# Kernel tuning notes

Measured on AMD Instinct MI355X. Metric: run time of the kernel, lower is better.

## Reference

```python
import jax, jax.numpy as jnp
import numpy as np

N = 102400   # total nodes (64 graphs x 1600 nodes)
G = 64       # graphs in batch
NPG = N // G
E = 1638400  # total edges (avg degree 16)
EPG = E // G


def _segmean(x, ids, num):
    s = jax.ops.segment_sum(x, ids, num_segments=num)
    c = jax.ops.segment_sum(jnp.ones((x.shape[0], 1), x.dtype), ids, num_segments=num)
    return s / jnp.maximum(c, 1.0)


def setup_inputs() -> dict:
    key = jax.random.key(0)
    ks = jax.random.split(key, 32)
    node_features = jax.random.normal(ks[0], (N, 60), jnp.float32)
    edge_features = jax.random.normal(ks[1], (E, 1), jnp.float32)
    node_graph = jnp.arange(N, dtype=jnp.int32) // NPG
    edge_graph = jnp.arange(E, dtype=jnp.int32) // EPG
    senders = edge_graph * NPG + jax.random.randint(ks[2], (E,), 0, NPG)
    receivers = edge_graph * NPG + jax.random.randint(ks[3], (E,), 0, NPG)

    def W(k, o, i):
        return (jax.random.normal(k, (o, i), jnp.float32) / np.sqrt(i)).astype(jnp.float32)

    def b(k, o):
        return (jax.random.uniform(k, (o,), jnp.float32) * 0.02 - 0.01).astype(jnp.float32)

    p = dict(
        node_features=node_features, edge_features=edge_features,
        senders=senders, receivers=receivers,
        node_graph=node_graph, edge_graph=edge_graph,
        # encoder: EdgeLinear(8, edge=1, sender=60)
        enc_Wee=W(ks[4], 8, 1), enc_Wes=W(ks[5], 8, 60), enc_be=b(ks[6], 8),
        # encoder: NodeLinear(16, incoming=8, node=60)
        enc_Wnn=W(ks[7], 16, 60), enc_Wni=W(ks[8], 16, 8), enc_bn=b(ks[9], 16),
        # encoder: GlobalLinear(4, edge=8, node=16)
        enc_Wge=W(ks[10], 4, 8), enc_Wgn=W(ks[11], 4, 16), enc_bg=b(ks[12], 4),
        # hidden: EdgeLinear(8, edge=8, sender=16, global=4)
        hid_Wee=W(ks[13], 8, 8), hid_Wes=W(ks[14], 8, 16), hid_Weg=W(ks[15], 8, 4), hid_be=b(ks[16], 8),
        # hidden: NodeLinear(16, node=16, incoming=8, global=4)
        hid_Wnn=W(ks[17], 16, 16), hid_Wni=W(ks[18], 16, 8), hid_Wng=W(ks[19], 16, 4), hid_bn=b(ks[20], 16),
        # hidden: GlobalLinear(4, edge=8, node=16, global=4)
        hid_Wge=W(ks[21], 4, 8), hid_Wgn=W(ks[22], 4, 16), hid_Wgg=W(ks[23], 4, 4), hid_bg=b(ks[24], 4),
        # readouts
        ro_Wn=W(ks[25], 1, 16), ro_bn=b(ks[26], 1),
        ro_Wg=W(ks[27], 1, 4), ro_bg=b(ks[28], 1),
    )
    return p


def reference(node_features, edge_features, senders, receivers, node_graph, edge_graph,
              enc_Wee, enc_Wes, enc_be, enc_Wnn, enc_Wni, enc_bn, enc_Wge, enc_Wgn, enc_bg,
              hid_Wee, hid_Wes, hid_Weg, hid_be, hid_Wnn, hid_Wni, hid_Wng, hid_bn,
              hid_Wge, hid_Wgn, hid_Wgg, hid_bg, ro_Wn, ro_bn, ro_Wg, ro_bg):
    hops = 1
    # ---- encoder GN block ----
    e = jax.nn.relu(edge_features @ enc_Wee.T + node_features[senders] @ enc_Wes.T + enc_be)  # [E,8]
    n = jax.nn.relu(node_features @ enc_Wnn.T + _segmean(e, receivers, N) @ enc_Wni.T + enc_bn)  # [N,16]
    g = jax.nn.relu(_segmean(e, edge_graph, G) @ enc_Wge.T + _segmean(n, node_graph, G) @ enc_Wgn.T + enc_bg)  # [G,4]
    # ---- hidden GN blocks (shared weights across hops) ----
    for _ in range(hops):
        e = jax.nn.relu(e @ hid_Wee.T + n[senders] @ hid_Wes.T + g[edge_graph] @ hid_Weg.T + hid_be)
        n = jax.nn.relu(n @ hid_Wnn.T + _segmean(e, receivers, N) @ hid_Wni.T + g[node_graph] @ hid_Wng.T + hid_bn)
        g = jax.nn.relu(_segmean(e, edge_graph, G) @ hid_Wge.T + _segmean(n, node_graph, G) @ hid_Wgn.T + g @ hid_Wgg.T + hid_bg)
    # ---- readouts ----
    nodes_out = jax.nn.sigmoid(n @ ro_Wn.T + ro_bn)    # [N,1]
    globals_out = jax.nn.sigmoid(g @ ro_Wg.T + ro_bg)  # [G,1]
    return nodes_out, globals_out
```

## Files before the change

kernel.cpp:

```cpp
#include <hip/hip_runtime.h>
#include <hip/hip_bf16.h>
#include <hip/hip_fp16.h>

#define NN   102400
#define NG   64
#define NPG  1600
#define NE   1638400
#define EPG  25600
#define EPC  (EPG / 4)

typedef unsigned int u32;
typedef unsigned short u16;

#define OFF_EDAT  0
#define OFF_SPROJ (NE)
#define OFF_PNN   (NE + 8 * NN)
#define OFF_DEG   (NE + 16 * NN)
#define OFF_START (NE + 17 * NN)
#define OFF_H4C   (NE + 18 * NN)
#define OFF_GS    (NE + 22 * NN)
#define GS_ESUM1 0
#define GS_NSUM1 512
#define GS_ESUM2 1536
#define GS_NSUM2 2048
#define GS_G1    3072
#define GS_GPE   3328
#define GS_GPN   3840

struct H8 { __half2 a, b, c, d; };
struct H4 { __half2 a, b; };

__device__ __forceinline__ void unpack8(const H8 v, float* o) {
    float2 t0 = __half22float2(v.a), t1 = __half22float2(v.b);
    float2 t2 = __half22float2(v.c), t3 = __half22float2(v.d);
    o[0]=t0.x; o[1]=t0.y; o[2]=t1.x; o[3]=t1.y; o[4]=t2.x; o[5]=t2.y; o[6]=t3.x; o[7]=t3.y;
}
__device__ __forceinline__ H8 pack8(const float* v) {
    H8 r;
    r.a = __floats2half2_rn(v[0], v[1]); r.b = __floats2half2_rn(v[2], v[3]);
    r.c = __floats2half2_rn(v[4], v[5]); r.d = __floats2half2_rn(v[6], v[7]);
    return r;
}
__device__ __forceinline__ H4 pack4(const float* v) {
    H4 r;
    r.a = __floats2half2_rn(v[0], v[1]); r.b = __floats2half2_rn(v[2], v[3]);
    return r;
}
__device__ __forceinline__ u16 f2bf(float f) {
    u32 u = __float_as_uint(f);
    return (u16)((u + 0x7fffu + ((u >> 16) & 1u)) >> 16);
}
__device__ __forceinline__ float wsum_par(float v) {
#pragma unroll
    for (int o = 2; o <= 32; o <<= 1) v += __shfl_xor(v, o);
    return v;
}
__device__ __forceinline__ float sigmoidf_(float x) { return 1.f / (1.f + expf(-x)); }

__global__ __launch_bounds__(512) void k_hist4(const int* __restrict__ rcv, int* __restrict__ h4) {
    __shared__ int h[NPG];
    const int g = blockIdx.x >> 2, c = blockIdx.x & 3;
    for (int i = threadIdx.x; i < NPG; i += 512) h[i] = 0;
    __syncthreads();
    const int base = g * EPG + c * EPC;
    for (int t = threadIdx.x; t < EPC; t += 512) atomicAdd(&h[rcv[base + t] - g * NPG], 1);
    __syncthreads();
    int* out = h4 + (size_t)(g * 4 + c) * NPG;
    for (int i = threadIdx.x; i < NPG; i += 512) out[i] = h[i];
}

__global__ __launch_bounds__(320) void k_scan(
    int* __restrict__ h4c, int* __restrict__ deg, int* __restrict__ start)
{
    __shared__ int part[320];
    const int g = blockIdx.x, tid = threadIdx.x;
    const int vb = tid * 5;
    int hc[5][4], d[5], pre[5];
    int ts = 0;
#pragma unroll
    for (int i = 0; i < 5; ++i) {
        const int v = vb + i;
#pragma unroll
        for (int c = 0; c < 4; ++c) hc[i][c] = h4c[(size_t)(g * 4 + c) * NPG + v];
        d[i] = hc[i][0] + hc[i][1] + hc[i][2] + hc[i][3];
        pre[i] = ts;
        ts += d[i];
    }
    part[tid] = ts;
    __syncthreads();
    for (int o = 1; o < 320; o <<= 1) {
        const int v = (tid >= o) ? part[tid - o] : 0;
        __syncthreads();
        part[tid] += v;
        __syncthreads();
    }
    const int off = g * EPG + part[tid] - ts;
#pragma unroll
    for (int i = 0; i < 5; ++i) {
        const int v = vb + i;
        const int st = off + pre[i];
        deg[g * NPG + v] = d[i];
        start[g * NPG + v] = st;
        int run = st;
#pragma unroll
        for (int c = 0; c < 4; ++c) {
            h4c[(size_t)(g * 4 + c) * NPG + v] = run;
            run += hc[i][c];
        }
    }
}

__global__ __launch_bounds__(512) void k_scatter4(
    const float* __restrict__ ef, const int* __restrict__ snd, const int* __restrict__ rcv,
    const int* __restrict__ h4c, u32* __restrict__ edat)
{
    __shared__ int cur[NPG];
    const int g = blockIdx.x >> 2, c = blockIdx.x & 3;
    const int* cb = h4c + (size_t)(g * 4 + c) * NPG;
    for (int i = threadIdx.x; i < NPG; i += 512) cur[i] = cb[i];
    __syncthreads();
    const int base = g * EPG + c * EPC;
    for (int t = threadIdx.x; t < EPC; t += 512) {
        const int e = base + t;
        const int r = rcv[e] - g * NPG;
        const int p = atomicAdd(&cur[r], 1);
        const u32 s = (u32)(snd[e] - g * NPG);
        edat[p] = (s << 16) | (u32)f2bf(ef[e]);
    }
}

__global__ __launch_bounds__(256) void k_node_pre(
    const float* __restrict__ nf,
    const float* __restrict__ Wes,
    const float* __restrict__ Wnn,
    const float* __restrict__ ebe, const float* __restrict__ ebn,
    __half* __restrict__ sproj, __half* __restrict__ pnn, float* __restrict__ gs)
{
    __shared__ float wE[480], wN[960];
    for (int i = threadIdx.x; i < 480; i += 256) wE[i] = Wes[i];
    for (int i = threadIdx.x; i < 960; i += 256) wN[i] = Wnn[i];
    if (blockIdx.x == 0) {
        for (int i = threadIdx.x; i < 3072; i += 256) gs[i] = 0.f;
    }
    __syncthreads();
    const int v = blockIdx.x * 256 + threadIdx.x;
    const float4* row = reinterpret_cast<const float4*>(nf + (size_t)v * 60);
    float x[60];
#pragma unroll
    for (int i = 0; i < 15; ++i) {
        const float4 a = row[i];
        x[4 * i] = a.x; x[4 * i + 1] = a.y; x[4 * i + 2] = a.z; x[4 * i + 3] = a.w;
    }
    float pes[8], pn[16];
#pragma unroll
    for (int j = 0; j < 8; ++j) pes[j] = ebe[j];
#pragma unroll
    for (int j = 0; j < 16; ++j) pn[j] = ebn[j];
#pragma unroll
    for (int k = 0; k < 60; ++k) {
        const float xv = x[k];
#pragma unroll
        for (int j = 0; j < 8; ++j)  pes[j] = fmaf(xv, wE[j * 60 + k], pes[j]);
#pragma unroll
        for (int j = 0; j < 16; ++j) pn[j]  = fmaf(xv, wN[j * 60 + k], pn[j]);
    }
    H8* sp = reinterpret_cast<H8*>(sproj) + (size_t)v * 2;
    sp[0] = pack8(pes);
    H8* pp = reinterpret_cast<H8*>(pnn) + (size_t)v * 2;
    pp[0] = pack8(pn); pp[1] = pack8(pn + 8);
}

__global__ __launch_bounds__(256) void k_enc(
    const int* __restrict__ deg, const int* __restrict__ start, const u32* __restrict__ edat,
    __half* __restrict__ sproj, __half* __restrict__ pnn,
    const float* __restrict__ eWee,
    const float* __restrict__ eWni,
    const float* __restrict__ hWes, const float* __restrict__ hWnn,
    float* __restrict__ esum, float* __restrict__ nsum)
{
    __shared__ float wNI[128], wES[128], wNN2[256];
    for (int i = threadIdx.x; i < 128; i += 256) { wNI[i] = eWni[i]; wES[i] = hWes[i]; }
    wNN2[threadIdx.x] = hWnn[threadIdx.x];
    __syncthreads();
    const int t = blockIdx.x * 256 + threadIdx.x;
    const int v = t >> 1, h = t & 1;
    const int g = v / NPG;
    float wee[8];
#pragma unroll
    for (int j = 0; j < 8; ++j) wee[j] = eWee[j];
    const int dg = deg[v];
    const int st = start[v];
    const int half0 = dg >> 1;
    int i = st + (h ? half0 : 0);
    const int iend = st + (h ? dg : half0);
    float m[8];
#pragma unroll
    for (int j = 0; j < 8; ++j) m[j] = 0.f;
    const H8* hb = reinterpret_cast<const H8*>(sproj) + (size_t)g * NPG * 2;

#define ENC_EDGE(W, A) { \
    const float f_ = __uint_as_float(((W) & 0xffffu) << 16); \
    float pv_[8]; unpack8((A), pv_); \
    _Pragma("unroll") \
    for (int j = 0; j < 8; ++j) m[j] += fmaxf(0.f, fmaf(f_, wee[j], pv_[j])); }

    for (; i + 4 <= iend; i += 4) {
        const u32 w0 = edat[i], w1 = edat[i + 1], w2v = edat[i + 2], w3v = edat[i + 3];
        const H8 A0 = hb[(size_t)(w0 >> 16) * 2];
        const H8 A1 = hb[(size_t)(w1 >> 16) * 2];
        const H8 A2 = hb[(size_t)(w2v >> 16) * 2];
        const H8 A3 = hb[(size_t)(w3v >> 16) * 2];
        ENC_EDGE(w0, A0) ENC_EDGE(w1, A1) ENC_EDGE(w2v, A2) ENC_EDGE(w3v, A3)
    }
    for (; i < iend; ++i) {
        const u32 w = edat[i];
        const H8 A = hb[(size_t)(w >> 16) * 2];
        ENC_EDGE(w, A)
    }
#undef ENC_EDGE

#pragma unroll
    for (int j = 0; j < 8; ++j) m[j] += __shfl_xor(m[j], 1);
#pragma unroll
    for (int j = 0; j < 8; ++j) {
        const float s = wsum_par(m[j]);
        if ((threadIdx.x & 63) == 0) atomicAdd(&esum[g * 8 + j], s);
    }
    const float ic = 1.f / fmaxf((float)dg, 1.f);
    float mk[8];
#pragma unroll
    for (int k = 0; k < 8; ++k) mk[k] = m[k] * ic;
    const H8* pp = reinterpret_cast<const H8*>(pnn) + (size_t)v * 2;
    float pn8[8]; unpack8(pp[h], pn8);
    float n1[8];
#pragma unroll
    for (int jj = 0; jj < 8; ++jj) {
        float x = pn8[jj];
#pragma unroll
        for (int k = 0; k < 8; ++k) x = fmaf(mk[k], wNI[(h * 8 + jj) * 8 + k], x);
        n1[jj] = fmaxf(0.f, x);
    }
    float n1o[8];
#pragma unroll
    for (int jj = 0; jj < 8; ++jj) n1o[jj] = __shfl_xor(n1[jj], 1);
    float full[16];
#pragma unroll
    for (int jj = 0; jj < 8; ++jj) {
        full[jj]     = h ? n1o[jj] : n1[jj];
        full[8 + jj] = h ? n1[jj]  : n1o[jj];
    }
    float pe4[4];
#pragma unroll
    for (int oo = 0; oo < 4; ++oo) {
        const int o = h * 4 + oo;
        float x = 0.f;
#pragma unroll
        for (int j = 0; j < 16; ++j) x = fmaf(full[j], wES[o * 16 + j], x);
        pe4[oo] = x;
    }
    *reinterpret_cast<H4*>(sproj + (size_t)v * 16 + 8 + h * 4) = pack4(pe4);
    float pw8[8];
#pragma unroll
    for (int oo = 0; oo < 8; ++oo) {
        const int o = h * 8 + oo;
        float x = 0.f;
#pragma unroll
        for (int j = 0; j < 16; ++j) x = fmaf(full[j], wNN2[o * 16 + j], x);
        pw8[oo] = x;
    }
    reinterpret_cast<H8*>(pnn)[(size_t)v * 2 + h] = pack8(pw8);
#pragma unroll
    for (int jj = 0; jj < 8; ++jj) {
        const float s = wsum_par(n1[jj]);
        if ((threadIdx.x & 63) == h) atomicAdd(&nsum[g * 16 + h * 8 + jj], s);
    }
}

__global__ void k_glob_enc(
    const float* __restrict__ esum1, const float* __restrict__ nsum1,
    const float* __restrict__ Wge, const float* __restrict__ Wgn, const float* __restrict__ bg,
    const float* __restrict__ hWeg, const float* __restrict__ hWng,
    float* __restrict__ g1, float* __restrict__ gpe, float* __restrict__ gpn)
{
    const int g = threadIdx.x;
    if (g >= NG) return;
    float gv[4];
#pragma unroll
    for (int o = 0; o < 4; ++o) {
        float x = bg[o];
#pragma unroll
        for (int k = 0; k < 8; ++k)  x = fmaf(esum1[g * 8 + k] * (1.f / EPG), Wge[o * 8 + k], x);
#pragma unroll
        for (int k = 0; k < 16; ++k) x = fmaf(nsum1[g * 16 + k] * (1.f / NPG), Wgn[o * 16 + k], x);
        gv[o] = fmaxf(0.f, x);
        g1[g * 4 + o] = gv[o];
    }
#pragma unroll
    for (int j = 0; j < 8; ++j) {
        float x = 0.f;
#pragma unroll
        for (int o = 0; o < 4; ++o) x = fmaf(gv[o], hWeg[j * 4 + o], x);
        gpe[g * 8 + j] = x;
    }
#pragma unroll
    for (int j = 0; j < 16; ++j) {
        float x = 0.f;
#pragma unroll
        for (int o = 0; o < 4; ++o) x = fmaf(gv[o], hWng[j * 4 + o], x);
        gpn[g * 16 + j] = x;
    }
}

__global__ __launch_bounds__(256) void k_hid(
    const int* __restrict__ deg, const int* __restrict__ start, const u32* __restrict__ edat,
    const __half* __restrict__ sproj, const __half* __restrict__ pnn,
    const float* __restrict__ eWee,
    const float* __restrict__ hWee, const float* __restrict__ hbe, const float* __restrict__ gpe,
    const float* __restrict__ hWni, const float* __restrict__ hbn, const float* __restrict__ gpn,
    const float* __restrict__ roWn, const float* __restrict__ robn,
    float* __restrict__ esum, float* __restrict__ nsum, float* __restrict__ outn)
{
    __shared__ float w2[64], wNI[128], rW[16];
    for (int i = threadIdx.x; i < 128; i += 256) wNI[i] = hWni[i];
    if (threadIdx.x < 64) w2[threadIdx.x] = hWee[threadIdx.x];
    if (threadIdx.x < 16) rW[threadIdx.x] = roWn[threadIdx.x];
    __syncthreads();
    const int t = blockIdx.x * 256 + threadIdx.x;
    const int v = t >> 1, h = t & 1;
    const int g = v / NPG;
    float wee[8], add2[8];
#pragma unroll
    for (int j = 0; j < 8; ++j) { wee[j] = eWee[j]; add2[j] = gpe[g * 8 + j] + hbe[j]; }
    const int dg = deg[v];
    const int st = start[v];
    const int half0 = dg >> 1;
    int i = st + (h ? half0 : 0);
    const int iend = st + (h ? dg : half0);
    float m2[8];
#pragma unroll
    for (int j = 0; j < 8; ++j) m2[j] = 0.f;
    const H8* hb = reinterpret_cast<const H8*>(sproj) + (size_t)g * NPG * 2;

#define HID_EDGE(W, A, B) { \
    const float f_ = __uint_as_float(((W) & 0xffffu) << 16); \
    float pv_[8], qv_[8]; unpack8((A), pv_); unpack8((B), qv_); \
    float e1_[8]; \
    _Pragma("unroll") \
    for (int j = 0; j < 8; ++j) e1_[j] = fmaxf(0.f, fmaf(f_, wee[j], pv_[j])); \
    _Pragma("unroll") \
    for (int j = 0; j < 8; ++j) { \
        float x_ = qv_[j] + add2[j]; \
        _Pragma("unroll") \
        for (int k = 0; k < 8; ++k) x_ = fmaf(e1_[k], w2[j * 8 + k], x_); \
        m2[j] += fmaxf(0.f, x_); } }

    for (; i + 4 <= iend; i += 4) {
        const u32 w0 = edat[i], w1 = edat[i + 1], w2v = edat[i + 2], w3v = edat[i + 3];
        const size_t s0 = (size_t)(w0 >> 16) * 2, s1 = (size_t)(w1 >> 16) * 2;
        const size_t s2 = (size_t)(w2v >> 16) * 2, s3 = (size_t)(w3v >> 16) * 2;
        const H8 A0 = hb[s0], B0 = hb[s0 + 1];
        const H8 A1 = hb[s1], B1 = hb[s1 + 1];
        const H8 A2 = hb[s2], B2 = hb[s2 + 1];
        const H8 A3 = hb[s3], B3 = hb[s3 + 1];
        HID_EDGE(w0, A0, B0) HID_EDGE(w1, A1, B1) HID_EDGE(w2v, A2, B2) HID_EDGE(w3v, A3, B3)
    }
    for (; i < iend; ++i) {
        const u32 w = edat[i];
        const size_t s = (size_t)(w >> 16) * 2;
        const H8 A = hb[s], B = hb[s + 1];
        HID_EDGE(w, A, B)
    }
#undef HID_EDGE

#pragma unroll
    for (int j = 0; j < 8; ++j) m2[j] += __shfl_xor(m2[j], 1);
#pragma unroll
    for (int j = 0; j < 8; ++j) {
        const float s = wsum_par(m2[j]);
        if ((threadIdx.x & 63) == 0) atomicAdd(&esum[g * 8 + j], s);
    }
    const float ic = 1.f / fmaxf((float)dg, 1.f);
    float mk[8];
#pragma unroll
    for (int k = 0; k < 8; ++k) mk[k] = m2[k] * ic;
    const H8* pp = reinterpret_cast<const H8*>(pnn) + (size_t)v * 2;
    float pn8[8]; unpack8(pp[h], pn8);
    float zp = 0.f;
    float n2[8];
#pragma unroll
    for (int jj = 0; jj < 8; ++jj) {
        const int j = h * 8 + jj;
        float x = pn8[jj] + gpn[g * 16 + j] + hbn[j];
#pragma unroll
        for (int k = 0; k < 8; ++k) x = fmaf(mk[k], wNI[j * 8 + k], x);
        n2[jj] = fmaxf(0.f, x);
        zp = fmaf(n2[jj], rW[j], zp);
    }
    const float z = zp + __shfl_xor(zp, 1);
    if (h == 0) outn[v] = sigmoidf_(z + robn[0]);
#pragma unroll
    for (int jj = 0; jj < 8; ++jj) {
        const float s = wsum_par(n2[jj]);
        if ((threadIdx.x & 63) == h) atomicAdd(&nsum[g * 16 + h * 8 + jj], s);
    }
}

__global__ void k_glob_hid(
    const float* __restrict__ esum2, const float* __restrict__ nsum2, const float* __restrict__ g1,
    const float* __restrict__ hWge, const float* __restrict__ hWgn,
    const float* __restrict__ hWgg, const float* __restrict__ hbg,
    const float* __restrict__ roWg, const float* __restrict__ robg,
    float* __restrict__ outg)
{
    const int g = threadIdx.x;
    if (g >= NG) return;
    float gv[4];
#pragma unroll
    for (int o = 0; o < 4; ++o) {
        float x = hbg[o];
#pragma unroll
        for (int k = 0; k < 8; ++k)  x = fmaf(esum2[g * 8 + k] * (1.f / EPG), hWge[o * 8 + k], x);
#pragma unroll
        for (int k = 0; k < 16; ++k) x = fmaf(nsum2[g * 16 + k] * (1.f / NPG), hWgn[o * 16 + k], x);
#pragma unroll
        for (int k = 0; k < 4; ++k)  x = fmaf(g1[g * 4 + k], hWgg[o * 4 + k], x);
        gv[o] = fmaxf(0.f, x);
    }
    float z = robg[0];
#pragma unroll
    for (int o = 0; o < 4; ++o) z = fmaf(gv[o], roWg[o], z);
    outg[g] = sigmoidf_(z);
}

extern "C" void kernel_launch(void* const* d_in, const int* in_sizes, int n_in,
                              void* d_out, int out_size, void* d_ws, size_t ws_size,
                              hipStream_t stream)
{
    const float* nf   = (const float*)d_in[0];
    const float* ef   = (const float*)d_in[1];
    const int*   snd  = (const int*)d_in[2];
    const int*   rcv  = (const int*)d_in[3];
    const float* eWee = (const float*)d_in[6];
    const float* eWes = (const float*)d_in[7];
    const float* ebe  = (const float*)d_in[8];
    const float* eWnn = (const float*)d_in[9];
    const float* eWni = (const float*)d_in[10];
    const float* ebn  = (const float*)d_in[11];
    const float* eWge = (const float*)d_in[12];
    const float* eWgn = (const float*)d_in[13];
    const float* ebg  = (const float*)d_in[14];
    const float* hWee = (const float*)d_in[15];
    const float* hWes = (const float*)d_in[16];
    const float* hWeg = (const float*)d_in[17];
    const float* hbe  = (const float*)d_in[18];
    const float* hWnn = (const float*)d_in[19];
    const float* hWni = (const float*)d_in[20];
    const float* hWng = (const float*)d_in[21];
    const float* hbn  = (const float*)d_in[22];
    const float* hWge = (const float*)d_in[23];
    const float* hWgn = (const float*)d_in[24];
    const float* hWgg = (const float*)d_in[25];
    const float* hbg  = (const float*)d_in[26];
    const float* roWn = (const float*)d_in[27];
    const float* robn = (const float*)d_in[28];
    const float* roWg = (const float*)d_in[29];
    const float* robg = (const float*)d_in[30];

    float*  ws    = (float*)d_ws;
    u32*    edat  = (u32*)(ws + OFF_EDAT);
    __half* sproj = (__half*)(ws + OFF_SPROJ);
    __half* pnn   = (__half*)(ws + OFF_PNN);
    int*    deg   = (int*)(ws + OFF_DEG);
    int*    start = (int*)(ws + OFF_START);
    int*    h4c   = (int*)(ws + OFF_H4C);
    float*  gs    = ws + OFF_GS;
    float* esum1 = gs + GS_ESUM1;
    float* nsum1 = gs + GS_NSUM1;
    float* esum2 = gs + GS_ESUM2;
    float* nsum2 = gs + GS_NSUM2;
    float* g1    = gs + GS_G1;
    float* gpe   = gs + GS_GPE;
    float* gpn   = gs + GS_GPN;
    float* out   = (float*)d_out;

    k_hist4<<<NG * 4, 512, 0, stream>>>(rcv, h4c);
    k_scan<<<NG, 320, 0, stream>>>(h4c, deg, start);
    k_scatter4<<<NG * 4, 512, 0, stream>>>(ef, snd, rcv, h4c, edat);
    k_node_pre<<<NN / 256, 256, 0, stream>>>(nf, eWes, eWnn, ebe, ebn, sproj, pnn, gs);
    k_enc<<<NN * 2 / 256, 256, 0, stream>>>(deg, start, edat, sproj, pnn,
                                            eWee, eWni, hWes, hWnn, esum1, nsum1);
    k_glob_enc<<<1, 64, 0, stream>>>(esum1, nsum1, eWge, eWgn, ebg, hWeg, hWng, g1, gpe, gpn);
    k_hid<<<NN * 2 / 256, 256, 0, stream>>>(deg, start, edat, sproj, pnn,
                                            eWee, hWee, hbe, gpe, hWni, hbn, gpn,
                                            roWn, robn, esum2, nsum2, out);
    k_glob_hid<<<1, 64, 0, stream>>>(esum2, nsum2, g1, hWge, hWgn, hWgg, hbg, roWg, robg, out + NN);
}
```

Before: 144.0 us.

## Stage per-graph sender projection tables in LDS for edge gathers

Reorganizes k_enc and k_hid so that each 512-thread block handles a 200-node chunk of a single graph. Each block first copies that graph's sender projection table (and, in k_hid, both halves of it) from global memory into shared memory, so the random per-edge gathers read LDS instead of global or L2. The cost is that every block redundantly reloads the whole per-graph table, and only 400 of the 512 threads in each block do work. The grid is also smaller, with larger LDS use per block, which may reduce occupancy and latency hiding.

```diff
diff --git a/kernel.cpp b/kernel.cpp
--- a/kernel.cpp
+++ b/kernel.cpp
@@ -8,6 +8,7 @@
 #define NE   1638400
 #define EPG  25600
 #define EPC  (EPG / 4)
+#define NPB  200
 
 typedef unsigned int u32;
 typedef unsigned short u16;
@@ -170,7 +171,7 @@
     pp[0] = pack8(pn); pp[1] = pack8(pn + 8);
 }
 
-__global__ __launch_bounds__(256) void k_enc(
+__global__ __launch_bounds__(512) void k_enc(
     const int* __restrict__ deg, const int* __restrict__ start, const u32* __restrict__ edat,
     __half* __restrict__ sproj, __half* __restrict__ pnn,
     const float* __restrict__ eWee,
@@ -178,25 +179,30 @@
     const float* __restrict__ hWes, const float* __restrict__ hWnn,
     float* __restrict__ esum, float* __restrict__ nsum)
 {
+    __shared__ float4 sA[NPG];
     __shared__ float wNI[128], wES[128], wNN2[256];
-    for (int i = threadIdx.x; i < 128; i += 256) { wNI[i] = eWni[i]; wES[i] = hWes[i]; }
-    wNN2[threadIdx.x] = hWnn[threadIdx.x];
-    __syncthreads();
-    const int t = blockIdx.x * 256 + threadIdx.x;
-    const int v = t >> 1, h = t & 1;
-    const int g = v / NPG;
+    const int g = blockIdx.x >> 3, c = blockIdx.x & 7;
+    const int tid = threadIdx.x;
+    const float4* f4sp = reinterpret_cast<const float4*>(sproj);
+    for (int i = tid; i < NPG; i += 512) sA[i] = f4sp[(size_t)(g * NPG + i) * 2];
+    for (int i = tid; i < 128; i += 512) { wNI[i] = eWni[i]; wES[i] = hWes[i]; }
+    for (int i = tid; i < 256; i += 512) wNN2[i] = hWnn[i];
+    __syncthreads();
     float wee[8];
 #pragma unroll
     for (int j = 0; j < 8; ++j) wee[j] = eWee[j];
-    const int dg = deg[v];
-    const int st = start[v];
+    const int local = tid >> 1, h = tid & 1;
+    const bool act = local < NPB;
+    const int v = g * NPG + c * NPB + (act ? local : 0);
+    const int dg = act ? deg[v] : 0;
+    const int st = act ? start[v] : 0;
     const int half0 = dg >> 1;
     int i = st + (h ? half0 : 0);
     const int iend = st + (h ? dg : half0);
     float m[8];
 #pragma unroll
     for (int j = 0; j < 8; ++j) m[j] = 0.f;
-    const H8* hb = reinterpret_cast<const H8*>(sproj) + (size_t)g * NPG * 2;
+    const H8* hb = reinterpret_cast<const H8*>(sA);
 
 #define ENC_EDGE(W, A) { \
     const float f_ = __uint_as_float(((W) & 0xffffu) << 16); \
@@ -206,15 +212,15 @@
 
     for (; i + 4 <= iend; i += 4) {
         const u32 w0 = edat[i], w1 = edat[i + 1], w2v = edat[i + 2], w3v = edat[i + 3];
-        const H8 A0 = hb[(size_t)(w0 >> 16) * 2];
-        const H8 A1 = hb[(size_t)(w1 >> 16) * 2];
-        const H8 A2 = hb[(size_t)(w2v >> 16) * 2];
-        const H8 A3 = hb[(size_t)(w3v >> 16) * 2];
+        const H8 A0 = hb[w0 >> 16];
+        const H8 A1 = hb[w1 >> 16];
+        const H8 A2 = hb[w2v >> 16];
+        const H8 A3 = hb[w3v >> 16];
         ENC_EDGE(w0, A0) ENC_EDGE(w1, A1) ENC_EDGE(w2v, A2) ENC_EDGE(w3v, A3)
     }
     for (; i < iend; ++i) {
         const u32 w = edat[i];
-        const H8 A = hb[(size_t)(w >> 16) * 2];
+        const H8 A = hb[w >> 16];
         ENC_EDGE(w, A)
     }
 #undef ENC_EDGE
@@ -224,14 +230,20 @@
 #pragma unroll
     for (int j = 0; j < 8; ++j) {
         const float s = wsum_par(m[j]);
-        if ((threadIdx.x & 63) == 0) atomicAdd(&esum[g * 8 + j], s);
+        if ((tid & 63) == 0) atomicAdd(&esum[g * 8 + j], s);
     }
     const float ic = 1.f / fmaxf((float)dg, 1.f);
     float mk[8];
 #pragma unroll
     for (int k = 0; k < 8; ++k) mk[k] = m[k] * ic;
-    const H8* pp = reinterpret_cast<const H8*>(pnn) + (size_t)v * 2;
-    float pn8[8]; unpack8(pp[h], pn8);
+    float pn8[8];
+    if (act) {
+        const H8* pp = reinterpret_cast<const H8*>(pnn) + (size_t)v * 2;
+        unpack8(pp[h], pn8);
+    } else {
+#pragma unroll
+        for (int jj = 0; jj < 8; ++jj) pn8[jj] = 0.f;
+    }
     float n1[8];
 #pragma unroll
     for (int jj = 0; jj < 8; ++jj) {
@@ -258,7 +270,7 @@
         for (int j = 0; j < 16; ++j) x = fmaf(full[j], wES[o * 16 + j], x);
         pe4[oo] = x;
     }
-    *reinterpret_cast<H4*>(sproj + (size_t)v * 16 + 8 + h * 4) = pack4(pe4);
+    if (act) *reinterpret_cast<H4*>(sproj + (size_t)v * 16 + 8 + h * 4) = pack4(pe4);
     float pw8[8];
 #pragma unroll
     for (int oo = 0; oo < 8; ++oo) {
@@ -268,11 +280,11 @@
         for (int j = 0; j < 16; ++j) x = fmaf(full[j], wNN2[o * 16 + j], x);
         pw8[oo] = x;
     }
-    reinterpret_cast<H8*>(pnn)[(size_t)v * 2 + h] = pack8(pw8);
+    if (act) reinterpret_cast<H8*>(pnn)[(size_t)v * 2 + h] = pack8(pw8);
 #pragma unroll
     for (int jj = 0; jj < 8; ++jj) {
         const float s = wsum_par(n1[jj]);
-        if ((threadIdx.x & 63) == h) atomicAdd(&nsum[g * 16 + h * 8 + jj], s);
+        if ((tid & 63) == h) atomicAdd(&nsum[g * 16 + h * 8 + jj], s);
     }
 }
 
@@ -311,7 +323,7 @@
     }
 }
 
-__global__ __launch_bounds__(256) void k_hid(
+__global__ __launch_bounds__(512) void k_hid(
     const int* __restrict__ deg, const int* __restrict__ start, const u32* __restrict__ edat,
     const __half* __restrict__ sproj, const __half* __restrict__ pnn,
     const float* __restrict__ eWee,
@@ -320,26 +332,31 @@
     const float* __restrict__ roWn, const float* __restrict__ robn,
     float* __restrict__ esum, float* __restrict__ nsum, float* __restrict__ outn)
 {
+    __shared__ float4 sAB[NPG * 2];
     __shared__ float w2[64], wNI[128], rW[16];
-    for (int i = threadIdx.x; i < 128; i += 256) wNI[i] = hWni[i];
-    if (threadIdx.x < 64) w2[threadIdx.x] = hWee[threadIdx.x];
-    if (threadIdx.x < 16) rW[threadIdx.x] = roWn[threadIdx.x];
-    __syncthreads();
-    const int t = blockIdx.x * 256 + threadIdx.x;
-    const int v = t >> 1, h = t & 1;
-    const int g = v / NPG;
+    const int g = blockIdx.x >> 3, c = blockIdx.x & 7;
+    const int tid = threadIdx.x;
+    const float4* f4sp = reinterpret_cast<const float4*>(sproj);
+    for (int i = tid; i < NPG * 2; i += 512) sAB[i] = f4sp[(size_t)g * NPG * 2 + i];
+    for (int i = tid; i < 128; i += 512) wNI[i] = hWni[i];
+    if (tid < 64) w2[tid] = hWee[tid];
+    if (tid < 16) rW[tid] = roWn[tid];
+    __syncthreads();
     float wee[8], add2[8];
 #pragma unroll
     for (int j = 0; j < 8; ++j) { wee[j] = eWee[j]; add2[j] = gpe[g * 8 + j] + hbe[j]; }
-    const int dg = deg[v];
-    const int st = start[v];
+    const int local = tid >> 1, h = tid & 1;
+    const bool act = local < NPB;
+    const int v = g * NPG + c * NPB + (act ? local : 0);
+    const int dg = act ? deg[v] : 0;
+    const int st = act ? start[v] : 0;
     const int half0 = dg >> 1;
     int i = st + (h ? half0 : 0);
     const int iend = st + (h ? dg : half0);
     float m2[8];
 #pragma unroll
     for (int j = 0; j < 8; ++j) m2[j] = 0.f;
-    const H8* hb = reinterpret_cast<const H8*>(sproj) + (size_t)g * NPG * 2;
+    const H8* hb = reinterpret_cast<const H8*>(sAB);
 
 #define HID_EDGE(W, A, B) { \
     const float f_ = __uint_as_float(((W) & 0xffffu) << 16); \
@@ -356,8 +373,8 @@
 
     for (; i + 4 <= iend; i += 4) {
         const u32 w0 = edat[i], w1 = edat[i + 1], w2v = edat[i + 2], w3v = edat[i + 3];
-        const size_t s0 = (size_t)(w0 >> 16) * 2, s1 = (size_t)(w1 >> 16) * 2;
-        const size_t s2 = (size_t)(w2v >> 16) * 2, s3 = (size_t)(w3v >> 16) * 2;
+        const int s0 = (int)(w0 >> 16) * 2, s1 = (int)(w1 >> 16) * 2;
+        const int s2 = (int)(w2v >> 16) * 2, s3 = (int)(w3v >> 16) * 2;
         const H8 A0 = hb[s0], B0 = hb[s0 + 1];
         const H8 A1 = hb[s1], B1 = hb[s1 + 1];
         const H8 A2 = hb[s2], B2 = hb[s2 + 1];
@@ -366,7 +383,7 @@
     }
     for (; i < iend; ++i) {
         const u32 w = edat[i];
-        const size_t s = (size_t)(w >> 16) * 2;
+        const int s = (int)(w >> 16) * 2;
         const H8 A = hb[s], B = hb[s + 1];
         HID_EDGE(w, A, B)
     }
@@ -377,14 +394,20 @@
 #pragma unroll
     for (int j = 0; j < 8; ++j) {
         const float s = wsum_par(m2[j]);
-        if ((threadIdx.x & 63) == 0) atomicAdd(&esum[g * 8 + j], s);
+        if ((tid & 63) == 0) atomicAdd(&esum[g * 8 + j], s);
     }
     const float ic = 1.f / fmaxf((float)dg, 1.f);
     float mk[8];
 #pragma unroll
     for (int k = 0; k < 8; ++k) mk[k] = m2[k] * ic;
-    const H8* pp = reinterpret_cast<const H8*>(pnn) + (size_t)v * 2;
-    float pn8[8]; unpack8(pp[h], pn8);
+    float pn8[8];
+    if (act) {
+        const H8* pp = reinterpret_cast<const H8*>(pnn) + (size_t)v * 2;
+        unpack8(pp[h], pn8);
+    } else {
+#pragma unroll
+        for (int jj = 0; jj < 8; ++jj) pn8[jj] = 0.f;
+    }
     float zp = 0.f;
     float n2[8];
 #pragma unroll
@@ -393,15 +416,15 @@
         float x = pn8[jj] + gpn[g * 16 + j] + hbn[j];
 #pragma unroll
         for (int k = 0; k < 8; ++k) x = fmaf(mk[k], wNI[j * 8 + k], x);
-        n2[jj] = fmaxf(0.f, x);
+        n2[jj] = act ? fmaxf(0.f, x) : 0.f;
         zp = fmaf(n2[jj], rW[j], zp);
     }
     const float z = zp + __shfl_xor(zp, 1);
-    if (h == 0) outn[v] = sigmoidf_(z + robn[0]);
+    if (act && h == 0) outn[v] = sigmoidf_(z + robn[0]);
 #pragma unroll
     for (int jj = 0; jj < 8; ++jj) {
         const float s = wsum_par(n2[jj]);
-        if ((threadIdx.x & 63) == h) atomicAdd(&nsum[g * 16 + h * 8 + jj], s);
+        if ((tid & 63) == h) atomicAdd(&nsum[g * 16 + h * 8 + jj], s);
     }
 }
 
@@ -487,11 +510,11 @@
     k_scan<<<NG, 320, 0, stream>>>(h4c, deg, start);
     k_scatter4<<<NG * 4, 512, 0, stream>>>(ef, snd, rcv, h4c, edat);
     k_node_pre<<<NN / 256, 256, 0, stream>>>(nf, eWes, eWnn, ebe, ebn, sproj, pnn, gs);
-    k_enc<<<NN * 2 / 256, 256, 0, stream>>>(deg, start, edat, sproj, pnn,
-                                            eWee, eWni, hWes, hWnn, esum1, nsum1);
+    k_enc<<<NG * 8, 512, 0, stream>>>(deg, start, edat, sproj, pnn,
+                                      eWee, eWni, hWes, hWnn, esum1, nsum1);
     k_glob_enc<<<1, 64, 0, stream>>>(esum1, nsum1, eWge, eWgn, ebg, hWeg, hWng, g1, gpe, gpn);
-    k_hid<<<NN * 2 / 256, 256, 0, stream>>>(deg, start, edat, sproj, pnn,
-                                            eWee, hWee, hbe, gpe, hWni, hbn, gpn,
-                                            roWn, robn, esum2, nsum2, out);
+    k_hid<<<NG * 8, 512, 0, stream>>>(deg, start, edat, sproj, pnn,
+                                      eWee, hWee, hbe, gpe, hWni, hbn, gpn,
+                                      roWn, robn, esum2, nsum2, out);
     k_glob_hid<<<1, 64, 0, stream>>>(esum2, nsum2, g1, hWge, hWgn, hWgg, hbg, roWg, robg, out + NN);
 }
```

New measurement: 157.7 us. +9.5%, slower.
